# Performance work log

Hardware: AMD Instinct MI355X
Metric: run time of the kernel (lower is better)

Reference implementation:

```python
import jax, jax.numpy as jnp
import numpy as np

KSIZE = 7
SIGMA = 3.0
ALPHA = 0.1
POS_VAL_FOR_ALL_NEG = 5.0
NEG_VAL_FOR_ALL_POS = -5.0


def _gauss_kernel():
    x = jnp.arange(KSIZE, dtype=jnp.float32) - (KSIZE - 1) / 2.0
    pdf = jnp.exp(-0.5 * (x / SIGMA) ** 2)
    return pdf / pdf.sum()


def _gaussian_blur(img):
    # img: (B, C, H, W); separable 7x7 gaussian, reflect padding (torchvision behavior)
    B, C, H, W = img.shape
    k = _gauss_kernel()
    pad = KSIZE // 2
    x = jnp.pad(img, ((0, 0), (0, 0), (pad, pad), (pad, pad)), mode='reflect')
    x = x.reshape(B * C, 1, H + 2 * pad, W + 2 * pad)
    kh = k.reshape(1, 1, KSIZE, 1)
    kw = k.reshape(1, 1, 1, KSIZE)
    x = jax.lax.conv_general_dilated(x, kh, (1, 1), 'VALID')
    x = jax.lax.conv_general_dilated(x, kw, (1, 1), 'VALID')
    return x.reshape(B, C, H, W)


def _dup_map(x, mask, fallback):
    # x, mask: (L,). Gather x[mask] (original order) then tile to length L.
    # Stable argsort puts True(=selected) positions first in original order.
    L = x.shape[0]
    cnt = mask.sum()
    order = jnp.argsort(jnp.logical_not(mask))  # selected indices first, stable
    idx = order[jnp.arange(L) % jnp.maximum(cnt, 1)]
    return jnp.where(cnt == 0, jnp.float32(fallback), x[idx])


_dup_vmapped = jax.vmap(_dup_map, in_axes=(0, 0, None))


def _bce_with_logits(x, y):
    # mean( max(x,0) - x*y + log1p(exp(-|x|)) ) == mean( softplus(x) - x*y )
    return jnp.mean(jnp.logaddexp(0.0, x) - x * y)


def _forward(inp, tgt):
    B, C, H, W = inp.shape
    aug_sim_target = (_gaussian_blur(tgt * 255.0) > 0).astype(jnp.float32)

    L = H * W
    x = inp.reshape(B * C, L)
    t = tgt.reshape(B * C, L)
    a = aug_sim_target.reshape(B * C, L)

    # duplicated_pos: gather input at target>0, tile; fallback +5 if no positives
    pos_mask = t > 0
    dup_pos = _dup_vmapped(x, pos_mask, POS_VAL_FOR_ALL_NEG)

    # duplicated_false_pos: prefer (input>0 & ~aug_pos); else all negatives; else -5
    aug_pos = a > 0
    fp_mask = jnp.logical_and(x > 0, jnp.logical_not(aug_pos))
    neg_mask = jnp.logical_not(aug_pos)
    cnt_fp = fp_mask.sum(axis=1, keepdims=True)
    chosen_mask = jnp.where(cnt_fp > 0, fp_mask, neg_mask)
    dup_fp = _dup_vmapped(x, chosen_mask, NEG_VAL_FOR_ALL_POS)

    sim = dup_pos * x
    aug_sim = dup_pos * dup_fp

    sim_loss = _bce_with_logits(sim, t) + _bce_with_logits(dup_pos, jnp.ones_like(x))
    aug_sim_loss = _bce_with_logits(aug_sim, jnp.zeros_like(x))
    return sim_loss + ALPHA * aug_sim_loss


def setup_inputs() -> dict:
    key = jax.random.key(0)
    k1, k2 = jax.random.split(key)
    B, C, H, W = 16, 3, 512, 512
    inp = jax.random.normal(k1, (B, C, H, W), dtype=jnp.float32)
    tgt = jax.random.randint(k2, (B, C, H, W), 0, 2).astype(jnp.float32)
    return {"input": inp, "target": tgt}


def reference(input, target):
    return _forward(input, target)
```

## Files before the change

kernel.cpp:

```cpp
#include <hip/hip_runtime.h>
#include <math.h>

constexpr int W = 512;
constexpr int HIMG = 512;
constexpr int L = 1 << 18;
constexpr int LOG2L = 18;
constexpr int TPB = 256;
constexpr int TILE = 2048;
constexpr int TILES_PER_ROW = L / TILE;
constexpr int WORDS_PER_ROW = L / 64;
constexpr int WORDS_PER_TILE = TILE / 64;

typedef unsigned long long ull;

__device__ __forceinline__ float softplus_f(float v) {
    return fmaxf(v, 0.0f) +
           0.6931471805599453f *
               __builtin_amdgcn_logf(1.0f + __builtin_amdgcn_exp2f(-fabsf(v) * 1.4426950408889634f));
}

__global__ void mask_kernel(const float* __restrict__ x, const float* __restrict__ t,
                            ull* __restrict__ maskT, ull* __restrict__ maskX, int nwords4) {
    int lane = threadIdx.x & 63;
    int waveId = (blockIdx.x * blockDim.x + threadIdx.x) >> 6;
    int nWaves = (gridDim.x * blockDim.x) >> 6;
    for (int wi = waveId; wi < nwords4; wi += nWaves) {
        int eb = wi * 256;
        int w0 = wi * 4;
        ull bt0 = __ballot(t[eb + lane] > 0.0f);
        ull bt1 = __ballot(t[eb + 64 + lane] > 0.0f);
        ull bt2 = __ballot(t[eb + 128 + lane] > 0.0f);
        ull bt3 = __ballot(t[eb + 192 + lane] > 0.0f);
        ull bx0 = __ballot(x[eb + lane] > 0.0f);
        ull bx1 = __ballot(x[eb + 64 + lane] > 0.0f);
        ull bx2 = __ballot(x[eb + 128 + lane] > 0.0f);
        ull bx3 = __ballot(x[eb + 192 + lane] > 0.0f);
        if (lane < 4) {
            ull v = (lane == 0) ? bt0 : (lane == 1) ? bt1 : (lane == 2) ? bt2 : bt3;
            maskT[w0 + lane] = v;
        } else if (lane < 8) {
            int k = lane - 4;
            ull v = (k == 0) ? bx0 : (k == 1) ? bx1 : (k == 2) ? bx2 : bx3;
            maskX[w0 + k] = v;
        }
    }
}

__device__ __forceinline__ ull hdil7(ull prev, ull cur, ull next) {
    ull r = cur;
    r |= (cur >> 1) | (next << 63);
    r |= (cur >> 2) | (next << 62);
    r |= (cur >> 3) | (next << 61);
    r |= (cur << 1) | (prev >> 63);
    r |= (cur << 2) | (prev >> 62);
    r |= (cur << 3) | (prev >> 61);
    return r;
}

__global__ void dilate_h_kernel(const ull* __restrict__ maskT, ull* __restrict__ maskH,
                                int nwords) {
    int w = blockIdx.x * blockDim.x + threadIdx.x;
    if (w >= nwords) return;
    int wcol = w & 7;
    ull cur = maskT[w];
    ull prev = wcol ? maskT[w - 1]
                    : ((((cur >> 1) & 1ull) << 63) | (((cur >> 2) & 1ull) << 62) |
                       (((cur >> 3) & 1ull) << 61));
    ull next = (wcol < 7) ? maskT[w + 1]
                          : (((cur >> 62) & 1ull) | (((cur >> 61) & 1ull) << 1) |
                             (((cur >> 60) & 1ull) << 2));
    maskH[w] = hdil7(prev, cur, next);
}

__global__ void dilate_v_kernel(const ull* __restrict__ maskH, ull* __restrict__ maskA,
                                int nwords) {
    int w = blockIdx.x * blockDim.x + threadIdx.x;
    if (w >= nwords) return;
    int wimg = w & (WORDS_PER_ROW - 1);
    int scan = wimg >> 3;
    int wcol = wimg & 7;
    int base = w - wimg;
    ull out = 0;
#pragma unroll
    for (int d = -3; d <= 3; ++d) {
        int ii = scan + d;
        ii = ii < 0 ? -ii : (ii > HIMG - 1 ? 2 * (HIMG - 1) - ii : ii);
        out |= maskH[base + ii * 8 + wcol];
    }
    maskA[w] = out;
}

__global__ void count_scan_kernel(const ull* __restrict__ maskT, const ull* __restrict__ maskX,
                                  const ull* __restrict__ maskA,
                                  int* __restrict__ oPos, int* __restrict__ oCh,
                                  int* __restrict__ rCp, int* __restrict__ rCc,
                                  ull* __restrict__ rMp, ull* __restrict__ rMc,
                                  int* __restrict__ rUseFp) {
    int r = blockIdx.x;
    int tid = threadIdx.x;
    int wb = r * WORDS_PER_ROW + tid * WORDS_PER_TILE;
    int p = 0, f = 0, n = 0;
#pragma unroll 4
    for (int k = 0; k < WORDS_PER_TILE; ++k) {
        ull wt = maskT[wb + k], wx = maskX[wb + k], wa = maskA[wb + k];
        p += __popcll(wt);
        f += __popcll(wx & ~wa);
        n += __popcll(~wa);
    }
    __shared__ int ssp[TILES_PER_ROW], ssf[TILES_PER_ROW], ssn[TILES_PER_ROW];
    ssp[tid] = p; ssf[tid] = f; ssn[tid] = n;
    __syncthreads();
    for (int off = 1; off < TILES_PER_ROW; off <<= 1) {
        int ap = tid >= off ? ssp[tid - off] : 0;
        int af = tid >= off ? ssf[tid - off] : 0;
        int an = tid >= off ? ssn[tid - off] : 0;
        __syncthreads();
        ssp[tid] += ap; ssf[tid] += af; ssn[tid] += an;
        __syncthreads();
    }
    int cp = ssp[TILES_PER_ROW - 1], cf = ssf[TILES_PER_ROW - 1], cn = ssn[TILES_PER_ROW - 1];
    bool useFp = cf > 0;
    int tile = r * TILES_PER_ROW + tid;
    oPos[tile] = ssp[tid] - p;
    oCh[tile] = useFp ? (ssf[tid] - f) : (ssn[tid] - n);
    if (tid == 0) {
        int cc = useFp ? cf : cn;
        rCp[r] = cp; rCc[r] = cc; rUseFp[r] = useFp ? 1 : 0;
        ull dp_ = (ull)(cp > 0 ? cp : 1);
        ull dc_ = (ull)(cc > 0 ? cc : 1);
        rMp[r] = ((1ull << 40) + dp_ - 1) / dp_;
        rMc[r] = ((1ull << 40) + dc_ - 1) / dc_;
    }
}

__global__ void scatter_kernel(const float* __restrict__ x,
                               const ull* __restrict__ maskT, const ull* __restrict__ maskX,
                               const ull* __restrict__ maskA,
                               const int* __restrict__ oPos, const int* __restrict__ oCh,
                               const int* __restrict__ rUseFp,
                               float* __restrict__ xp, float* __restrict__ xf) {
    int tile = blockIdx.x;
    int tid = threadIdx.x;
    int r = tile >> 7;
    bool useFp = rUseFp[r] != 0;
    int widx = tile * WORDS_PER_TILE + (tid >> 3);
    int shift = (tid & 7) * 8;
    ull wa = maskA[widx];
    unsigned bT = (unsigned)(maskT[widx] >> shift) & 0xFF;
    unsigned bCh = useFp ? ((unsigned)((maskX[widx] & ~wa) >> shift) & 0xFF)
                         : ((unsigned)((~wa) >> shift) & 0xFF);
    const float4* x4 = (const float4*)x;
    int b4 = tile * (TILE / 4) + tid * 2;
    float4 a = x4[b4], b = x4[b4 + 1];
    float xv[8] = {a.x, a.y, a.z, a.w, b.x, b.y, b.z, b.w};
    int p = __popc(bT), c = __popc(bCh);
    __shared__ int s[TPB];
    int v = p | (c << 16);
    s[tid] = v;
    __syncthreads();
    for (int off = 1; off < TPB; off <<= 1) {
        int add = tid >= off ? s[tid - off] : 0;
        __syncthreads();
        s[tid] += add;
        __syncthreads();
    }
    int excl = s[tid] - v;
    int rL = r << LOG2L;
    int pw = rL + oPos[tile] + (excl & 0xFFFF);
    int cw = rL + oCh[tile] + (excl >> 16);
#pragma unroll
    for (int e = 0; e < 8; ++e) {
        if ((bT >> e) & 1) xp[pw++] = xv[e];
        if ((bCh >> e) & 1) xf[cw++] = xv[e];
    }
}

__global__ void loss_kernel(const float* __restrict__ x, const ull* __restrict__ maskT,
                            const float* __restrict__ xp, const float* __restrict__ xf,
                            const int* __restrict__ rCp, const int* __restrict__ rCc,
                            const ull* __restrict__ rMp, const ull* __restrict__ rMc,
                            double* __restrict__ acc, int n4) {
    int tid = threadIdx.x;
    int stride = gridDim.x * blockDim.x;
    float local = 0.0f;
    const float4* x4 = (const float4*)x;
    for (int i4 = blockIdx.x * blockDim.x + tid; i4 < n4; i4 += stride) {
        int g = i4 << 2;
        int r = g >> LOG2L;
        unsigned l = (unsigned)(g & (L - 1));
        float4 xv = x4[i4];
        unsigned tb = (unsigned)(maskT[g >> 6] >> (g & 63)) & 0xFu;
        int cp = rCp[r], cc = rCc[r];
        int rL = r << LOG2L;
        float dps[4], dfs[4];
        if (cp > 0) {
            ull M = rMp[r];
            unsigned d = (unsigned)cp;
            unsigned q = (unsigned)(((ull)l * M) >> 40);
            unsigned m0 = l - q * d;
            unsigned m1 = m0 + 1; if (m1 == d) m1 = 0;
            unsigned m2 = m1 + 1; if (m2 == d) m2 = 0;
            unsigned m3 = m2 + 1; if (m3 == d) m3 = 0;
            dps[0] = xp[rL + m0]; dps[1] = xp[rL + m1];
            dps[2] = xp[rL + m2]; dps[3] = xp[rL + m3];
        } else {
            dps[0] = dps[1] = dps[2] = dps[3] = 5.0f;
        }
        if (cc > 0) {
            ull M = rMc[r];
            unsigned d = (unsigned)cc;
            unsigned q = (unsigned)(((ull)l * M) >> 40);
            unsigned m0 = l - q * d;
            unsigned m1 = m0 + 1; if (m1 == d) m1 = 0;
            unsigned m2 = m1 + 1; if (m2 == d) m2 = 0;
            unsigned m3 = m2 + 1; if (m3 == d) m3 = 0;
            dfs[0] = xf[rL + m0]; dfs[1] = xf[rL + m1];
            dfs[2] = xf[rL + m2]; dfs[3] = xf[rL + m3];
        } else {
            dfs[0] = dfs[1] = dfs[2] = dfs[3] = -5.0f;
        }
        float xs[4] = {xv.x, xv.y, xv.z, xv.w};
#pragma unroll
        for (int k = 0; k < 4; ++k) {
            float sim = dps[k] * xs[k];
            float e = softplus_f(sim) + softplus_f(-dps[k]) + 0.1f * softplus_f(dps[k] * dfs[k]);
            if ((tb >> k) & 1) e -= sim;
            local += e;
        }
    }
    __shared__ double sd[TPB];
    sd[tid] = (double)local;
    __syncthreads();
    for (int off = TPB / 2; off > 0; off >>= 1) {
        if (tid < off) sd[tid] += sd[tid + off];
        __syncthreads();
    }
    if (tid == 0) atomicAdd(acc, sd[0]);
}

__global__ void finalize_kernel(const double* __restrict__ acc, float* __restrict__ out,
                                int ntot) {
    out[0] = (float)(acc[0] / (double)ntot);
}

extern "C" void kernel_launch(void* const* d_in, const int* in_sizes, int n_in,
                              void* d_out, int out_size, void* d_ws, size_t ws_size,
                              hipStream_t stream) {
    const float* x = (const float*)d_in[0];
    const float* t = (const float*)d_in[1];
    float* out = (float*)d_out;

    int ntot = in_sizes[0];
    int R = ntot >> LOG2L;
    int numTiles = ntot / TILE;
    int nwords = ntot / 64;
    int nwords4 = nwords / 4;

    char* ws = (char*)d_ws;
    size_t off = 0;
    auto alloc = [&](size_t bytes) {
        size_t p = off;
        off = (off + bytes + 255) & ~(size_t)255;
        return (void*)(ws + p);
    };
    double* acc = (double*)alloc(sizeof(double));
    ull* maskT = (ull*)alloc((size_t)nwords * 8);
    ull* maskX = (ull*)alloc((size_t)nwords * 8);
    ull* maskH = (ull*)alloc((size_t)nwords * 8);
    ull* maskA = (ull*)alloc((size_t)nwords * 8);
    int* oPos = (int*)alloc(numTiles * sizeof(int));
    int* oCh  = (int*)alloc(numTiles * sizeof(int));
    int* rCp = (int*)alloc(R * sizeof(int));
    int* rCc = (int*)alloc(R * sizeof(int));
    int* rUseFp = (int*)alloc(R * sizeof(int));
    ull* rMp = (ull*)alloc(R * sizeof(ull));
    ull* rMc = (ull*)alloc(R * sizeof(ull));
    float* xp = (float*)alloc((size_t)ntot * sizeof(float));
    float* xf = (float*)alloc((size_t)ntot * sizeof(float));

    (void)hipMemsetAsync(acc, 0, sizeof(double), stream);

    mask_kernel<<<768, TPB, 0, stream>>>(x, t, maskT, maskX, nwords4);
    dilate_h_kernel<<<nwords / TPB, TPB, 0, stream>>>(maskT, maskH, nwords);
    dilate_v_kernel<<<nwords / TPB, TPB, 0, stream>>>(maskH, maskA, nwords);
    count_scan_kernel<<<R, TILES_PER_ROW, 0, stream>>>(maskT, maskX, maskA, oPos, oCh,
                                                       rCp, rCc, rMp, rMc, rUseFp);
    scatter_kernel<<<numTiles, TPB, 0, stream>>>(x, maskT, maskX, maskA, oPos, oCh, rUseFp,
                                                 xp, xf);
    loss_kernel<<<2048, TPB, 0, stream>>>(x, maskT, xp, xf, rCp, rCc, rMp, rMc, acc,
                                          ntot / 4);
    finalize_kernel<<<1, 1, 0, stream>>>(acc, out, ntot);
}
```

Baseline: 194.2 us.

## Fuse mask and horizontal dilation, coalesce count scan, row-blocked loss

Merges mask construction and horizontal dilation into one kernel that handles one full image scanline per wave, and folds the accumulator zeroing into that kernel instead of a separate memset. Rewrites the count/scan kernel to read masks coalesced with 256 threads and stage per-word popcounts in shared memory. Restructures the loss kernel so each block covers a fixed chunk of one row, hoisting per-row parameters out of the loop. The aim is fewer launches, less mask-buffer traffic and better coalescing, at the cost of more register use in the fused kernel.

```diff
diff --git a/kernel.cpp b/kernel.cpp
--- a/kernel.cpp
+++ b/kernel.cpp
@@ -10,6 +10,9 @@
 constexpr int TILES_PER_ROW = L / TILE;
 constexpr int WORDS_PER_ROW = L / 64;
 constexpr int WORDS_PER_TILE = TILE / 64;
+constexpr int LBLK = 32;
+constexpr int CHUNK = L / LBLK;
+constexpr int LIT = CHUNK / (TPB * 4);
 
 typedef unsigned long long ull;
 
@@ -17,33 +20,6 @@
     return fmaxf(v, 0.0f) +
            0.6931471805599453f *
                __builtin_amdgcn_logf(1.0f + __builtin_amdgcn_exp2f(-fabsf(v) * 1.4426950408889634f));
-}
-
-__global__ void mask_kernel(const float* __restrict__ x, const float* __restrict__ t,
-                            ull* __restrict__ maskT, ull* __restrict__ maskX, int nwords4) {
-    int lane = threadIdx.x & 63;
-    int waveId = (blockIdx.x * blockDim.x + threadIdx.x) >> 6;
-    int nWaves = (gridDim.x * blockDim.x) >> 6;
-    for (int wi = waveId; wi < nwords4; wi += nWaves) {
-        int eb = wi * 256;
-        int w0 = wi * 4;
-        ull bt0 = __ballot(t[eb + lane] > 0.0f);
-        ull bt1 = __ballot(t[eb + 64 + lane] > 0.0f);
-        ull bt2 = __ballot(t[eb + 128 + lane] > 0.0f);
-        ull bt3 = __ballot(t[eb + 192 + lane] > 0.0f);
-        ull bx0 = __ballot(x[eb + lane] > 0.0f);
-        ull bx1 = __ballot(x[eb + 64 + lane] > 0.0f);
-        ull bx2 = __ballot(x[eb + 128 + lane] > 0.0f);
-        ull bx3 = __ballot(x[eb + 192 + lane] > 0.0f);
-        if (lane < 4) {
-            ull v = (lane == 0) ? bt0 : (lane == 1) ? bt1 : (lane == 2) ? bt2 : bt3;
-            maskT[w0 + lane] = v;
-        } else if (lane < 8) {
-            int k = lane - 4;
-            ull v = (k == 0) ? bx0 : (k == 1) ? bx1 : (k == 2) ? bx2 : bx3;
-            maskX[w0 + k] = v;
-        }
-    }
 }
 
 __device__ __forceinline__ ull hdil7(ull prev, ull cur, ull next) {
@@ -57,19 +33,45 @@
     return r;
 }
 
-__global__ void dilate_h_kernel(const ull* __restrict__ maskT, ull* __restrict__ maskH,
-                                int nwords) {
-    int w = blockIdx.x * blockDim.x + threadIdx.x;
-    if (w >= nwords) return;
-    int wcol = w & 7;
-    ull cur = maskT[w];
-    ull prev = wcol ? maskT[w - 1]
-                    : ((((cur >> 1) & 1ull) << 63) | (((cur >> 2) & 1ull) << 62) |
-                       (((cur >> 3) & 1ull) << 61));
-    ull next = (wcol < 7) ? maskT[w + 1]
-                          : (((cur >> 62) & 1ull) | (((cur >> 61) & 1ull) << 1) |
-                             (((cur >> 60) & 1ull) << 2));
-    maskH[w] = hdil7(prev, cur, next);
+template <typename T>
+__device__ __forceinline__ T sel8(const T* a, int k) {
+    return k == 0 ? a[0] : k == 1 ? a[1] : k == 2 ? a[2] : k == 3 ? a[3]
+         : k == 4 ? a[4] : k == 5 ? a[5] : k == 6 ? a[6] : a[7];
+}
+
+__global__ void mask_dilh_kernel(const float* __restrict__ x, const float* __restrict__ t,
+                                 ull* __restrict__ maskT, ull* __restrict__ maskX,
+                                 ull* __restrict__ maskH, double* __restrict__ acc,
+                                 int nScan) {
+    if (blockIdx.x == 0 && threadIdx.x == 0) acc[0] = 0.0;
+    int lane = threadIdx.x & 63;
+    int wave = (blockIdx.x * TPB + threadIdx.x) >> 6;
+    int nW = (gridDim.x * TPB) >> 6;
+    for (int s = wave; s < nScan; s += nW) {
+        int eb = s << 9;
+        ull wt[8], wx[8], h[8];
+#pragma unroll
+        for (int k = 0; k < 8; ++k) {
+            wt[k] = __ballot(t[eb + k * 64 + lane] > 0.0f);
+            wx[k] = __ballot(x[eb + k * 64 + lane] > 0.0f);
+        }
+#pragma unroll
+        for (int k = 0; k < 8; ++k) {
+            ull cur = wt[k];
+            ull prev = k ? wt[k - 1]
+                         : ((((cur >> 1) & 1ull) << 63) | (((cur >> 2) & 1ull) << 62) |
+                            (((cur >> 3) & 1ull) << 61));
+            ull next = (k < 7) ? wt[k + 1]
+                               : (((cur >> 62) & 1ull) | (((cur >> 61) & 1ull) << 1) |
+                                  (((cur >> 60) & 1ull) << 2));
+            h[k] = hdil7(prev, cur, next);
+        }
+        int w0 = s << 3;
+        int k = lane & 7;
+        if (lane < 8) maskT[w0 + k] = sel8(wt, k);
+        else if (lane < 16) maskX[w0 + k] = sel8(wx, k);
+        else if (lane < 24) maskH[w0 + k] = sel8(h, k);
+    }
 }
 
 __global__ void dilate_v_kernel(const ull* __restrict__ maskH, ull* __restrict__ maskA,
@@ -98,38 +100,50 @@
                                   int* __restrict__ rUseFp) {
     int r = blockIdx.x;
     int tid = threadIdx.x;
-    int wb = r * WORDS_PER_ROW + tid * WORDS_PER_TILE;
-    int p = 0, f = 0, n = 0;
-#pragma unroll 4
-    for (int k = 0; k < WORDS_PER_TILE; ++k) {
-        ull wt = maskT[wb + k], wx = maskX[wb + k], wa = maskA[wb + k];
-        p += __popcll(wt);
-        f += __popcll(wx & ~wa);
-        n += __popcll(~wa);
-    }
+    __shared__ unsigned char pw[WORDS_PER_ROW], fw[WORDS_PER_ROW], nw[WORDS_PER_ROW];
+    int base = r * WORDS_PER_ROW;
+#pragma unroll
+    for (int c = 0; c < WORDS_PER_ROW / TPB; ++c) {
+        int w = c * TPB + tid;
+        ull wt = maskT[base + w], wx = maskX[base + w], wa = maskA[base + w];
+        pw[w] = (unsigned char)__popcll(wt);
+        fw[w] = (unsigned char)__popcll(wx & ~wa);
+        nw[w] = (unsigned char)(64 - __popcll(wa));
+    }
+    __syncthreads();
     __shared__ int ssp[TILES_PER_ROW], ssf[TILES_PER_ROW], ssn[TILES_PER_ROW];
-    ssp[tid] = p; ssf[tid] = f; ssn[tid] = n;
+    int myp = 0, myf = 0, myn = 0;
+    if (tid < TILES_PER_ROW) {
+        int wb = tid * WORDS_PER_TILE;
+#pragma unroll 8
+        for (int k = 0; k < WORDS_PER_TILE; ++k) {
+            myp += pw[wb + k]; myf += fw[wb + k]; myn += nw[wb + k];
+        }
+        ssp[tid] = myp; ssf[tid] = myf; ssn[tid] = myn;
+    }
     __syncthreads();
     for (int off = 1; off < TILES_PER_ROW; off <<= 1) {
-        int ap = tid >= off ? ssp[tid - off] : 0;
-        int af = tid >= off ? ssf[tid - off] : 0;
-        int an = tid >= off ? ssn[tid - off] : 0;
-        __syncthreads();
-        ssp[tid] += ap; ssf[tid] += af; ssn[tid] += an;
-        __syncthreads();
-    }
-    int cp = ssp[TILES_PER_ROW - 1], cf = ssf[TILES_PER_ROW - 1], cn = ssn[TILES_PER_ROW - 1];
-    bool useFp = cf > 0;
-    int tile = r * TILES_PER_ROW + tid;
-    oPos[tile] = ssp[tid] - p;
-    oCh[tile] = useFp ? (ssf[tid] - f) : (ssn[tid] - n);
-    if (tid == 0) {
-        int cc = useFp ? cf : cn;
-        rCp[r] = cp; rCc[r] = cc; rUseFp[r] = useFp ? 1 : 0;
-        ull dp_ = (ull)(cp > 0 ? cp : 1);
-        ull dc_ = (ull)(cc > 0 ? cc : 1);
-        rMp[r] = ((1ull << 40) + dp_ - 1) / dp_;
-        rMc[r] = ((1ull << 40) + dc_ - 1) / dc_;
+        int ap = 0, af = 0, an = 0;
+        bool act = (tid < TILES_PER_ROW && tid >= off);
+        if (act) { ap = ssp[tid - off]; af = ssf[tid - off]; an = ssn[tid - off]; }
+        __syncthreads();
+        if (act) { ssp[tid] += ap; ssf[tid] += af; ssn[tid] += an; }
+        __syncthreads();
+    }
+    if (tid < TILES_PER_ROW) {
+        int cp = ssp[TILES_PER_ROW - 1], cf = ssf[TILES_PER_ROW - 1], cn = ssn[TILES_PER_ROW - 1];
+        bool useFp = cf > 0;
+        int tile = r * TILES_PER_ROW + tid;
+        oPos[tile] = ssp[tid] - myp;
+        oCh[tile] = useFp ? (ssf[tid] - myf) : (ssn[tid] - myn);
+        if (tid == 0) {
+            int cc = useFp ? cf : cn;
+            rCp[r] = cp; rCc[r] = cc; rUseFp[r] = useFp ? 1 : 0;
+            ull dp_ = (ull)(cp > 0 ? cp : 1);
+            ull dc_ = (ull)(cc > 0 ? cc : 1);
+            rMp[r] = ((1ull << 40) + dp_ - 1) / dp_;
+            rMc[r] = ((1ull << 40) + dc_ - 1) / dc_;
+        }
     }
 }
 
@@ -175,47 +189,48 @@
     }
 }
 
-__global__ void loss_kernel(const float* __restrict__ x, const ull* __restrict__ maskT,
-                            const float* __restrict__ xp, const float* __restrict__ xf,
-                            const int* __restrict__ rCp, const int* __restrict__ rCc,
-                            const ull* __restrict__ rMp, const ull* __restrict__ rMc,
-                            double* __restrict__ acc, int n4) {
-    int tid = threadIdx.x;
-    int stride = gridDim.x * blockDim.x;
+__global__ __launch_bounds__(TPB)
+void loss_kernel(const float* __restrict__ x, const ull* __restrict__ maskT,
+                 const float* __restrict__ xp, const float* __restrict__ xf,
+                 const int* __restrict__ rCp, const int* __restrict__ rCc,
+                 const ull* __restrict__ rMp, const ull* __restrict__ rMc,
+                 double* __restrict__ acc) {
+    int r = blockIdx.x >> 5;
+    int cb = (blockIdx.x & 31) * CHUNK;
+    int rL = r << LOG2L;
+    int cp = rCp[r], cc = rCc[r];
+    ull Mp = rMp[r], Mc = rMc[r];
+    const float4* x4 = (const float4*)(x + rL + cb);
+    const float* xpr = xp + rL;
+    const float* xfr = xf + rL;
+    const ull* mtr = maskT + (rL >> 6);
     float local = 0.0f;
-    const float4* x4 = (const float4*)x;
-    for (int i4 = blockIdx.x * blockDim.x + tid; i4 < n4; i4 += stride) {
-        int g = i4 << 2;
-        int r = g >> LOG2L;
-        unsigned l = (unsigned)(g & (L - 1));
-        float4 xv = x4[i4];
-        unsigned tb = (unsigned)(maskT[g >> 6] >> (g & 63)) & 0xFu;
-        int cp = rCp[r], cc = rCc[r];
-        int rL = r << LOG2L;
+#pragma unroll
+    for (int it = 0; it < LIT; ++it) {
+        int o4 = it * TPB + threadIdx.x;
+        unsigned l = (unsigned)(cb + (o4 << 2));
+        float4 xv = x4[o4];
+        unsigned tb = (unsigned)(mtr[l >> 6] >> (l & 63)) & 0xFu;
         float dps[4], dfs[4];
         if (cp > 0) {
-            ull M = rMp[r];
             unsigned d = (unsigned)cp;
-            unsigned q = (unsigned)(((ull)l * M) >> 40);
+            unsigned q = (unsigned)(((ull)l * Mp) >> 40);
             unsigned m0 = l - q * d;
             unsigned m1 = m0 + 1; if (m1 == d) m1 = 0;
             unsigned m2 = m1 + 1; if (m2 == d) m2 = 0;
             unsigned m3 = m2 + 1; if (m3 == d) m3 = 0;
-            dps[0] = xp[rL + m0]; dps[1] = xp[rL + m1];
-            dps[2] = xp[rL + m2]; dps[3] = xp[rL + m3];
+            dps[0] = xpr[m0]; dps[1] = xpr[m1]; dps[2] = xpr[m2]; dps[3] = xpr[m3];
         } else {
             dps[0] = dps[1] = dps[2] = dps[3] = 5.0f;
         }
         if (cc > 0) {
-            ull M = rMc[r];
             unsigned d = (unsigned)cc;
-            unsigned q = (unsigned)(((ull)l * M) >> 40);
+            unsigned q = (unsigned)(((ull)l * Mc) >> 40);
             unsigned m0 = l - q * d;
             unsigned m1 = m0 + 1; if (m1 == d) m1 = 0;
             unsigned m2 = m1 + 1; if (m2 == d) m2 = 0;
             unsigned m3 = m2 + 1; if (m3 == d) m3 = 0;
-            dfs[0] = xf[rL + m0]; dfs[1] = xf[rL + m1];
-            dfs[2] = xf[rL + m2]; dfs[3] = xf[rL + m3];
+            dfs[0] = xfr[m0]; dfs[1] = xfr[m1]; dfs[2] = xfr[m2]; dfs[3] = xfr[m3];
         } else {
             dfs[0] = dfs[1] = dfs[2] = dfs[3] = -5.0f;
         }
@@ -229,6 +244,7 @@
         }
     }
     __shared__ double sd[TPB];
+    int tid = threadIdx.x;
     sd[tid] = (double)local;
     __syncthreads();
     for (int off = TPB / 2; off > 0; off >>= 1) {
@@ -254,7 +270,7 @@
     int R = ntot >> LOG2L;
     int numTiles = ntot / TILE;
     int nwords = ntot / 64;
-    int nwords4 = nwords / 4;
+    int nScan = ntot / W;
 
     char* ws = (char*)d_ws;
     size_t off = 0;
@@ -278,16 +294,12 @@
     float* xp = (float*)alloc((size_t)ntot * sizeof(float));
     float* xf = (float*)alloc((size_t)ntot * sizeof(float));
 
-    (void)hipMemsetAsync(acc, 0, sizeof(double), stream);
-
-    mask_kernel<<<768, TPB, 0, stream>>>(x, t, maskT, maskX, nwords4);
-    dilate_h_kernel<<<nwords / TPB, TPB, 0, stream>>>(maskT, maskH, nwords);
+    mask_dilh_kernel<<<1536, TPB, 0, stream>>>(x, t, maskT, maskX, maskH, acc, nScan);
     dilate_v_kernel<<<nwords / TPB, TPB, 0, stream>>>(maskH, maskA, nwords);
-    count_scan_kernel<<<R, TILES_PER_ROW, 0, stream>>>(maskT, maskX, maskA, oPos, oCh,
-                                                       rCp, rCc, rMp, rMc, rUseFp);
+    count_scan_kernel<<<R, TPB, 0, stream>>>(maskT, maskX, maskA, oPos, oCh,
+                                             rCp, rCc, rMp, rMc, rUseFp);
     scatter_kernel<<<numTiles, TPB, 0, stream>>>(x, maskT, maskX, maskA, oPos, oCh, rUseFp,
                                                  xp, xf);
-    loss_kernel<<<2048, TPB, 0, stream>>>(x, maskT, xp, xf, rCp, rCc, rMp, rMc, acc,
-                                          ntot / 4);
+    loss_kernel<<<R * LBLK, TPB, 0, stream>>>(x, maskT, xp, xf, rCp, rCc, rMp, rMc, acc);
     finalize_kernel<<<1, 1, 0, stream>>>(acc, out, ntot);
 }
```

New measurement: 178.4 us. 1.09x faster.
